# Kernel tuning notes

Hardware: AMD Instinct MI355X
Metric: run time of the kernel (lower is better)

## Reference

```python
import jax, jax.numpy as jnp
import numpy as np


def crf_log_likelihood(logits, tags, mask, transitions, start_trans, end_trans):
    """AllenNLP-style linear-chain CRF log-likelihood, summed over the batch.
    logits: [B,T,K] float, tags: [B,T] int, mask: [B,T] float (1=valid).
    include_start_end_transitions=True.
    """
    B, T, K = logits.shape
    lt = jnp.transpose(logits, (1, 0, 2))          # [T,B,K]
    mt = jnp.transpose(mask, (1, 0))               # [T,B]
    tt = jnp.transpose(tags, (1, 0))               # [T,B]

    # ---- partition function (forward algorithm) ----
    alpha0 = start_trans + lt[0]                   # [B,K]

    def part_step(alpha, xs):
        emit, m = xs                               # emit [B,K], m [B]
        # inner[b,i,j] = alpha[b,i] + transitions[i,j] + emit[b,j]
        inner = alpha[:, :, None] + emit[:, None, :] + transitions[None, :, :]
        new_alpha = jax.nn.logsumexp(inner, axis=1)
        alpha = new_alpha * m[:, None] + alpha * (1.0 - m[:, None])
        return alpha, None

    alpha, _ = jax.lax.scan(part_step, alpha0, (lt[1:], mt[1:]))
    log_denominator = jax.nn.logsumexp(alpha + end_trans, axis=1)  # [B]

    # ---- joint (gold-path) score ----
    score0 = start_trans[tt[0]]                    # [B]

    def joint_step(score, xs):
        cur, nxt, emit, m_cur, m_nxt = xs
        trans_s = transitions[cur, nxt]                                   # [B]
        emit_s = jnp.take_along_axis(emit, cur[:, None], axis=1)[:, 0]    # [B]
        return score + trans_s * m_nxt + emit_s * m_cur, None

    score, _ = jax.lax.scan(joint_step, score0,
                            (tt[:-1], tt[1:], lt[:-1], mt[:-1], mt[1:]))
    last_idx = (jnp.sum(mt, axis=0) - 1.0).astype(jnp.int32)              # [B]
    last_tags = tt[last_idx, jnp.arange(B)]                               # [B]
    last_emit = jnp.take_along_axis(lt[-1], last_tags[:, None], axis=1)[:, 0]
    score = score + end_trans[last_tags] + last_emit * mt[-1]
    return jnp.sum(score - log_denominator)


def setup_inputs() -> dict:
    key = jax.random.key(0)
    ks = jax.random.split(key, 6)
    B, T, D, K = 64, 512, 768, 21
    vectors = jax.random.normal(ks[0], (B, T, D), dtype=jnp.float32)
    targets = jax.random.randint(ks[1], (B, T), 0, K, dtype=jnp.int32)
    mask = jnp.ones((B, T), dtype=jnp.int32)
    # Linear(input_dim, n_classes)
    W = jax.random.normal(ks[2], (K, D), dtype=jnp.float32) * (1.0 / np.sqrt(D))
    b = jax.random.normal(ks[3], (K,), dtype=jnp.float32) * 0.01
    transitions = jax.random.normal(ks[4], (K, K), dtype=jnp.float32) * 0.1
    se = jax.random.normal(ks[5], (2, K), dtype=jnp.float32) * 0.1
    return {"vectors": vectors, "targets": targets, "mask": mask,
            "W": W, "b": b, "transitions": transitions,
            "start_trans": se[0], "end_trans": se[1]}


def reference(vectors, targets, mask, W, b, transitions, start_trans, end_trans):
    logits = jnp.einsum('btd,kd->btk', vectors, W) + b     # proj
    maskf = mask.astype(logits.dtype)
    ll = crf_log_likelihood(logits, targets, maskf, transitions, start_trans, end_trans)
    loss = -ll / jnp.sum(maskf)
    return loss, logits
```

## Files before the change

kernel.cpp:

```cpp
#include <hip/hip_runtime.h>

#define B_ 64
#define T_ 512
#define D_ 768
#define K_ 21
#define NCHUNK 32
#define CLEN 16
#define GSTRIDE 448
#define LOG21 3.0445224377234229965f
#define WSTRIDE 776
#define ASTRIDE 136

using f16x8 = __attribute__((ext_vector_type(8))) _Float16;
using h16x4 = __attribute__((ext_vector_type(4))) _Float16;
using f32x4 = __attribute__((ext_vector_type(4))) float;

__global__ __launch_bounds__(256) void proj_kernel(
    const float* __restrict__ A,
    const float* __restrict__ W,
    const float* __restrict__ bias,
    float* __restrict__ out)
{
    __shared__ _Float16 Wh[K_ * WSTRIDE];
    __shared__ _Float16 Ah[2][64 * ASTRIDE];
    const int tid  = threadIdx.x;
    const int lane = tid & 63;
    const int w    = tid >> 6;
    const int m    = lane & 15;
    const int quad = lane >> 4;
    const size_t row0 = (size_t)blockIdx.x * 64;

    {
        const float4* Wg = (const float4*)W;
        for (int i = tid; i < K_ * D_ / 4; i += 256) {
            const float4 v = Wg[i];
            const int fi = i * 4;
            const int r = fi / D_;
            const int c = fi - r * D_;
            h16x4 h;
            h[0] = (_Float16)v.x; h[1] = (_Float16)v.y;
            h[2] = (_Float16)v.z; h[3] = (_Float16)v.w;
            *(h16x4*)(&Wh[r * WSTRIDE + c]) = h;
        }
    }

    float4 pf[8];
    #pragma unroll
    for (int j = 0; j < 8; ++j) {
        const int i = tid + j * 256;
        const int r = i >> 5, c4 = i & 31;
        pf[j] = *(const float4*)(A + (row0 + r) * D_ + c4 * 4);
    }
    #pragma unroll
    for (int j = 0; j < 8; ++j) {
        const int i = tid + j * 256;
        const int r = i >> 5, c4 = i & 31;
        h16x4 h;
        h[0] = (_Float16)pf[j].x; h[1] = (_Float16)pf[j].y;
        h[2] = (_Float16)pf[j].z; h[3] = (_Float16)pf[j].w;
        *(h16x4*)(&Ah[0][r * ASTRIDE + c4 * 4]) = h;
    }
    __syncthreads();

    f32x4 acc0 = {0.f, 0.f, 0.f, 0.f};
    f32x4 acc1 = {0.f, 0.f, 0.f, 0.f};
    const int n1 = (16 + m < K_) ? 16 + m : K_ - 1;

    for (int kt = 0; kt < 6; ++kt) {
        if (kt < 5) {
            #pragma unroll
            for (int j = 0; j < 8; ++j) {
                const int i = tid + j * 256;
                const int r = i >> 5, c4 = i & 31;
                pf[j] = *(const float4*)(A + (row0 + r) * D_ + (kt + 1) * 128 + c4 * 4);
            }
        }
        const _Float16* Ab = Ah[kt & 1];
        #pragma unroll
        for (int s = 0; s < 4; ++s) {
            const f16x8 af = *(const f16x8*)(&Ab[(w * 16 + m) * ASTRIDE + s * 32 + quad * 8]);
            const f16x8 bf = *(const f16x8*)(&Wh[m * WSTRIDE + kt * 128 + s * 32 + quad * 8]);
            const f16x8 cf = *(const f16x8*)(&Wh[n1 * WSTRIDE + kt * 128 + s * 32 + quad * 8]);
            acc0 = __builtin_amdgcn_mfma_f32_16x16x32_f16(af, bf, acc0, 0, 0, 0);
            acc1 = __builtin_amdgcn_mfma_f32_16x16x32_f16(af, cf, acc1, 0, 0, 0);
        }
        if (kt < 5) {
            _Float16* Aw = Ah[(kt + 1) & 1];
            #pragma unroll
            for (int j = 0; j < 8; ++j) {
                const int i = tid + j * 256;
                const int r = i >> 5, c4 = i & 31;
                h16x4 h;
                h[0] = (_Float16)pf[j].x; h[1] = (_Float16)pf[j].y;
                h[2] = (_Float16)pf[j].z; h[3] = (_Float16)pf[j].w;
                *(h16x4*)(&Aw[r * ASTRIDE + c4 * 4]) = h;
            }
        }
        __syncthreads();
    }

    const size_t rbase = row0 + w * 16 + quad * 4;
    {
        const float bb = bias[m];
        float* o = out + 1 + rbase * K_ + m;
        #pragma unroll
        for (int r = 0; r < 4; ++r) o[(size_t)r * K_] = acc0[r] + bb;
    }
    const int col2 = 16 + m;
    if (col2 < K_) {
        const float bb = bias[col2];
        float* o = out + 1 + rbase * K_ + col2;
        #pragma unroll
        for (int r = 0; r < 4; ++r) o[(size_t)r * K_] = acc1[r] + bb;
    }
}

__global__ __launch_bounds__(64, 1) void chunk_kernel(
    const float* __restrict__ outF,
    const int*   __restrict__ mask,
    const float* __restrict__ trans,
    float* __restrict__ G,
    float* __restrict__ SC)
{
    __shared__ float M0[441], M1[441];
    __shared__ float sET[441];
    __shared__ float em[CLEN * K_];
    __shared__ float smx[CLEN];
    __shared__ int   smask[CLEN];

    const int c = blockIdx.x;
    const int b = blockIdx.y;
    const int lane = threadIdx.x;
    const int t0 = c * CLEN + 1;
    const int nst = min(CLEN, T_ - t0);
    const int i_ = lane / 3;
    const int jg = lane - i_ * 3;
    const bool act = lane < 63;

    const float* lg = outF + 1 + (size_t)b * T_ * K_;
    for (int idx = lane; idx < nst * K_; idx += 64) em[idx] = lg[t0 * K_ + idx];
    if (lane < nst) smask[lane] = mask[b * T_ + t0 + lane];
    for (int idx = lane; idx < 441; idx += 64) {
        M0[idx] = (idx % 22 == 0) ? 1.0f : 0.0f;
        sET[idx] = __expf(trans[idx]);
    }
    __syncthreads();

    if (lane < nst) {
        float mx = -1e30f;
        for (int j = 0; j < K_; ++j) mx = fmaxf(mx, em[lane * K_ + j]);
        smx[lane] = mx;
    }
    __syncthreads();
    for (int idx = lane; idx < nst * K_; idx += 64)
        em[idx] = __expf(em[idx] - smx[idx / K_]) * (1.0f / 21.0f);

    float ETc[K_ * 7];
    if (act) {
        #pragma unroll
        for (int mm = 0; mm < K_; ++mm) {
            #pragma unroll
            for (int q = 0; q < 7; ++q)
                ETc[mm * 7 + q] = sET[mm * K_ + jg * 7 + q];
        }
    }
    __syncthreads();

    int cur = 0;
    for (int s = 0; s < nst; ++s) {
        if (smask[s] != 0) {
            const float* Mr = cur ? M1 : M0;
            float*       Mw = cur ? M0 : M1;
            float facc[7] = {0.f,0.f,0.f,0.f,0.f,0.f,0.f};
            if (act) {
                #pragma unroll
                for (int mm = 0; mm < K_; ++mm) {
                    const float lm = Mr[i_ * K_ + mm];
                    #pragma unroll
                    for (int q = 0; q < 7; ++q)
                        facc[q] = fmaf(lm, ETc[mm * 7 + q], facc[q]);
                }
            }
            __syncthreads();
            if (act) {
                #pragma unroll
                for (int q = 0; q < 7; ++q)
                    Mw[i_ * K_ + jg * 7 + q] = facc[q] * em[s * K_ + jg * 7 + q];
            }
            __syncthreads();
            cur ^= 1;
        }
    }

    float* Gc = G + (size_t)(b * NCHUNK + c) * GSTRIDE;
    const float* Mf = cur ? M1 : M0;
    for (int idx = lane; idx < 441; idx += 64) Gc[idx] = Mf[idx];
    if (lane == 0) {
        float sc = 0.0f;
        for (int s = 0; s < nst; ++s)
            if (smask[s] != 0) sc += smx[s] + LOG21;
        SC[b * NCHUNK + c] = sc;
    }
}

__global__ __launch_bounds__(256) void scan_kernel(
    const float* __restrict__ outF,
    const int*   __restrict__ tags,
    const int*   __restrict__ mask,
    const float* __restrict__ trans,
    const float* __restrict__ startT,
    const float* __restrict__ endT,
    const float* __restrict__ G,
    const float* __restrict__ SC,
    float* __restrict__ ll,
    float* __restrict__ msum)
{
    __shared__ float sG[NCHUNK * GSTRIDE];
    __shared__ float sm[T_];
    __shared__ int   st[T_];
    __shared__ float part[8];
    const int tid = threadIdx.x;
    const int lane = tid & 63;
    const int w = tid >> 6;
    const int b = blockIdx.x;
    const float* lg = outF + 1 + (size_t)b * T_ * K_;

    {
        const float4* Gf4 = (const float4*)(G + (size_t)b * NCHUNK * GSTRIDE);
        float4* dst = (float4*)sG;
        for (int i = tid; i < NCHUNK * GSTRIDE / 4; i += 256) dst[i] = Gf4[i];
    }
    for (int t = tid; t < T_; t += 256) {
        sm[t] = (float)mask[b * T_ + t];
        st[t] = tags[b * T_ + t];
    }
    __syncthreads();

    float logZ = 0.0f;
    if (w == 0) {
        const float scv = (lane < NCHUNK) ? SC[b * NCHUNK + lane] : 0.0f;
        const int jc = min(lane, K_ - 1);
        float v = (lane < K_) ? __expf(startT[lane] + lg[lane]) : 0.0f;
        float C = 0.0f;
        for (int c = 0; c < NCHUNK; ++c) {
            const float* Gc = sG + c * GSTRIDE;
            float a0 = 0.f, a1 = 0.f, a2 = 0.f;
            #pragma unroll
            for (int i = 0; i < K_; i += 3) {
                a0 = fmaf(__shfl(v, i,     64), Gc[i * K_ + jc],       a0);
                a1 = fmaf(__shfl(v, i + 1, 64), Gc[(i + 1) * K_ + jc], a1);
                a2 = fmaf(__shfl(v, i + 2, 64), Gc[(i + 2) * K_ + jc], a2);
            }
            const float s = a0 + a1 + a2;
            const float s0 = __shfl(s, 0, 64);
            v = s / s0;
            C += __logf(s0) + __shfl(scv, c, 64);
        }
        float term = (lane < K_) ? v * __expf(endT[lane]) : 0.0f;
        #pragma unroll
        for (int off = 16; off >= 1; off >>= 1) term += __shfl_xor(term, off, 64);
        term += __shfl_xor(term, 32, 64);
        logZ = C + __logf(term);
    } else {
        float sc = 0.0f, ms = 0.0f;
        for (int t = tid - 64; t < T_; t += 192) {
            const float mt = sm[t];
            ms += mt;
            if (t < T_ - 1) {
                const int ct = st[t], nt2 = st[t + 1];
                sc += trans[ct * K_ + nt2] * sm[t + 1] + lg[t * K_ + ct] * mt;
            }
        }
        #pragma unroll
        for (int off = 32; off >= 1; off >>= 1) {
            sc += __shfl_xor(sc, off, 64);
            ms += __shfl_xor(ms, off, 64);
        }
        if (lane == 0) { part[w] = sc; part[4 + w] = ms; }
    }
    __syncthreads();

    if (tid == 0) {
        float sc = part[1] + part[2] + part[3];
        float ms = part[5] + part[6] + part[7];
        const int lastIdx = (int)ms - 1;
        const int lastTag = st[lastIdx];
        sc += startT[st[0]] + endT[lastTag] + lg[(T_ - 1) * K_ + lastTag] * sm[T_ - 1];
        ll[b]   = sc - logZ;
        msum[b] = ms;
    }
}

__global__ __launch_bounds__(64) void fin_kernel(
    const float* __restrict__ ll, const float* __restrict__ msum,
    float* __restrict__ outF)
{
    const int lane = threadIdx.x;
    float l = ll[lane];
    float m = msum[lane];
    #pragma unroll
    for (int off = 32; off >= 1; off >>= 1) {
        l += __shfl_xor(l, off, 64);
        m += __shfl_xor(m, off, 64);
    }
    if (lane == 0) outF[0] = -l / m;
}

__global__ __launch_bounds__(64) void crf_kernel(
    const float* __restrict__ outF,
    const int*   __restrict__ tags,
    const int*   __restrict__ mask,
    const float* __restrict__ trans,
    const float* __restrict__ startT,
    const float* __restrict__ endT,
    float* __restrict__ ws)
{
    __shared__ float se[T_ * K_];
    __shared__ float sm[T_];
    __shared__ int   st[T_];
    const int b = blockIdx.x;
    const int lane = threadIdx.x;

    const float* lg = outF + 1 + (size_t)b * T_ * K_;
    for (int i = lane; i < T_ * K_; i += 64) se[i] = lg[i];
    for (int t = lane; t < T_; t += 64) {
        sm[t] = (float)mask[b * T_ + t];
        st[t] = tags[b * T_ + t];
    }
    __syncthreads();

    const int jc = lane < K_ ? lane : K_ - 1;
    float ET[K_];
    #pragma unroll
    for (int i = 0; i < K_; ++i) ET[i] = __expf(trans[i * K_ + jc]);

    float a0   = startT[jc] + se[jc];
    float r0   = __shfl(a0, 0, 64);
    float aRel = a0 - r0;
    float C    = r0;

    for (int t = 1; t < T_; ++t) {
        if (sm[t] != 0.0f) {
            float e = __expf(aRel);
            float s = 0.0f;
            #pragma unroll
            for (int i = 0; i < K_; ++i)
                s = fmaf(__shfl(e, i, 64), ET[i], s);
            float raw = __logf(s) + se[t * K_ + jc];
            float rr  = __shfl(raw, 0, 64);
            aRel = raw - rr;
            C   += rr;
        }
    }

    float contrib = (lane < K_) ? __expf(aRel + endT[jc]) : 0.0f;
    #pragma unroll
    for (int off = 32; off >= 1; off >>= 1) contrib += __shfl_xor(contrib, off, 64);
    const float logZ = C + __logf(contrib);

    float sc = 0.0f, ms = 0.0f;
    for (int t = lane; t < T_; t += 64) {
        const float mt = sm[t];
        ms += mt;
        if (t < T_ - 1) {
            const int ct = st[t], nt2 = st[t + 1];
            sc += trans[ct * K_ + nt2] * sm[t + 1] + se[t * K_ + ct] * mt;
        }
    }
    #pragma unroll
    for (int off = 32; off >= 1; off >>= 1) {
        sc += __shfl_xor(sc, off, 64);
        ms += __shfl_xor(ms, off, 64);
    }
    if (lane == 0) {
        const int lastIdx = (int)ms - 1;
        const int lastTag = st[lastIdx];
        sc += startT[st[0]] + endT[lastTag] + se[(T_ - 1) * K_ + lastTag] * sm[T_ - 1];
        ws[b]      = sc - logZ;
        ws[B_ + b] = ms;
    }
}

extern "C" void kernel_launch(void* const* d_in, const int* in_sizes, int n_in,
                              void* d_out, int out_size, void* d_ws, size_t ws_size,
                              hipStream_t stream) {
    const float* A     = (const float*)d_in[0];
    const int*   tags  = (const int*)  d_in[1];
    const int*   mask  = (const int*)  d_in[2];
    const float* W     = (const float*)d_in[3];
    const float* bias  = (const float*)d_in[4];
    const float* trans = (const float*)d_in[5];
    const float* stT   = (const float*)d_in[6];
    const float* enT   = (const float*)d_in[7];
    float* outF = (float*)d_out;
    float* ws   = (float*)d_ws;

    proj_kernel<<<512, 256, 0, stream>>>(A, W, bias, outF);

    const size_t gFloats  = (size_t)B_ * NCHUNK * GSTRIDE;
    const size_t scOff    = gFloats;
    const size_t llOff    = gFloats + (size_t)B_ * NCHUNK;
    const size_t msOff    = llOff + B_;
    const size_t needBytes = (msOff + B_) * sizeof(float);

    if (ws_size >= needBytes) {
        float* G   = ws;
        float* SC  = ws + scOff;
        float* llp = ws + llOff;
        float* msv = ws + msOff;
        chunk_kernel<<<dim3(NCHUNK, B_), 64, 0, stream>>>(outF, mask, trans, G, SC);
        scan_kernel<<<B_, 256, 0, stream>>>(outF, tags, mask, trans, stT, enT, G, SC, llp, msv);
        fin_kernel<<<1, 64, 0, stream>>>(llp, msv, outF);
    } else {
        crf_kernel<<<B_, 64, 0, stream>>>(outF, tags, mask, trans, stT, enT, ws);
        fin_kernel<<<1, 64, 0, stream>>>(ws, ws + B_, outF);
    }
}
```

Measured before the change: 207.0 us.

## Fuse CRF chunk transfer-matrix computation into projection epilogue and fold final reduction

Each projection wave computes its 16-timestep CRF transfer matrix directly from the logits it just produced. The logits are staged in reused LDS, so the separate chunk kernel and its global reload of logits go away. Synchronization inside the chunk recurrence becomes wave-local waits instead of block barriers. The final loss reduction moves into the scan kernel through an atomic last-block counter, which removes the fin kernel launch. The cost is extra LDS, extra work in the projection epilogue, and a chunk grouping shifted by one timestep, which makes the projection kernel heavier.

```diff
diff --git a/kernel.cpp b/kernel.cpp
--- a/kernel.cpp
+++ b/kernel.cpp
@@ -5,30 +5,52 @@
 #define D_ 768
 #define K_ 21
 #define NCHUNK 32
-#define CLEN 16
 #define GSTRIDE 448
 #define LOG21 3.0445224377234229965f
 #define WSTRIDE 776
 #define ASTRIDE 136
 
+#define WAVE_SYNC() asm volatile("s_waitcnt lgkmcnt(0)" ::: "memory")
+
 using f16x8 = __attribute__((ext_vector_type(8))) _Float16;
 using h16x4 = __attribute__((ext_vector_type(4))) _Float16;
 using f32x4 = __attribute__((ext_vector_type(4))) float;
 
-__global__ __launch_bounds__(256) void proj_kernel(
+__global__ __launch_bounds__(256, 2) void proj_chunk_kernel(
     const float* __restrict__ A,
     const float* __restrict__ W,
     const float* __restrict__ bias,
-    float* __restrict__ out)
+    const int*   __restrict__ mask,
+    const float* __restrict__ trans,
+    float* __restrict__ out,
+    float* __restrict__ G,
+    float* __restrict__ SC,
+    int*   __restrict__ cnt)
 {
     __shared__ _Float16 Wh[K_ * WSTRIDE];
     __shared__ _Float16 Ah[2][64 * ASTRIDE];
+    __shared__ float    sET[441];
     const int tid  = threadIdx.x;
     const int lane = tid & 63;
     const int w    = tid >> 6;
     const int m    = lane & 15;
     const int quad = lane >> 4;
     const size_t row0 = (size_t)blockIdx.x * 64;
+    const bool gmode = (G != nullptr);
+
+    if (gmode && blockIdx.x == 0 && tid == 0) *cnt = 0;
+
+    const int b     = blockIdx.x >> 3;
+    const int chunk = ((blockIdx.x & 7) << 2) + w;
+    const int t0    = chunk * 16;
+
+    unsigned int mbits = 0;
+    if (gmode) {
+        const int mv = (lane < 16) ? mask[b * T_ + t0 + lane] : 0;
+        const unsigned long long mb = __ballot(mv != 0);
+        mbits = (unsigned int)(mb & 0xFFFFull);
+        if (chunk == 0) mbits &= ~1u;
+    }
 
     {
         const float4* Wg = (const float4*)W;
@@ -43,6 +65,7 @@
             *(h16x4*)(&Wh[r * WSTRIDE + c]) = h;
         }
     }
+    for (int i = tid; i < 441; i += 256) sET[i] = __expf(trans[i]);
 
     float4 pf[8];
     #pragma unroll
@@ -99,62 +122,53 @@
         __syncthreads();
     }
 
+    float* const cb  = reinterpret_cast<float*>(&Ah[0][0]) + w * 1280;
+    float* const M0p = cb;
+    float* const M1p = cb + 441;
+    float* const em  = cb + 882;
+    float* const smx = cb + 1218;
+
     const size_t rbase = row0 + w * 16 + quad * 4;
     {
         const float bb = bias[m];
         float* o = out + 1 + rbase * K_ + m;
         #pragma unroll
-        for (int r = 0; r < 4; ++r) o[(size_t)r * K_] = acc0[r] + bb;
+        for (int r = 0; r < 4; ++r) {
+            const float v = acc0[r] + bb;
+            o[(size_t)r * K_] = v;
+            if (gmode) em[(quad * 4 + r) * K_ + m] = v;
+        }
     }
     const int col2 = 16 + m;
     if (col2 < K_) {
         const float bb = bias[col2];
         float* o = out + 1 + rbase * K_ + col2;
         #pragma unroll
-        for (int r = 0; r < 4; ++r) o[(size_t)r * K_] = acc1[r] + bb;
-    }
-}
-
-__global__ __launch_bounds__(64, 1) void chunk_kernel(
-    const float* __restrict__ outF,
-    const int*   __restrict__ mask,
-    const float* __restrict__ trans,
-    float* __restrict__ G,
-    float* __restrict__ SC)
-{
-    __shared__ float M0[441], M1[441];
-    __shared__ float sET[441];
-    __shared__ float em[CLEN * K_];
-    __shared__ float smx[CLEN];
-    __shared__ int   smask[CLEN];
-
-    const int c = blockIdx.x;
-    const int b = blockIdx.y;
-    const int lane = threadIdx.x;
-    const int t0 = c * CLEN + 1;
-    const int nst = min(CLEN, T_ - t0);
-    const int i_ = lane / 3;
-    const int jg = lane - i_ * 3;
-    const bool act = lane < 63;
-
-    const float* lg = outF + 1 + (size_t)b * T_ * K_;
-    for (int idx = lane; idx < nst * K_; idx += 64) em[idx] = lg[t0 * K_ + idx];
-    if (lane < nst) smask[lane] = mask[b * T_ + t0 + lane];
-    for (int idx = lane; idx < 441; idx += 64) {
-        M0[idx] = (idx % 22 == 0) ? 1.0f : 0.0f;
-        sET[idx] = __expf(trans[idx]);
-    }
-    __syncthreads();
-
-    if (lane < nst) {
+        for (int r = 0; r < 4; ++r) {
+            const float v = acc1[r] + bb;
+            o[(size_t)r * K_] = v;
+            if (gmode) em[(quad * 4 + r) * K_ + col2] = v;
+        }
+    }
+    if (!gmode) return;
+    WAVE_SYNC();
+
+    if (lane < 16) {
         float mx = -1e30f;
+        #pragma unroll
         for (int j = 0; j < K_; ++j) mx = fmaxf(mx, em[lane * K_ + j]);
         smx[lane] = mx;
     }
-    __syncthreads();
-    for (int idx = lane; idx < nst * K_; idx += 64)
-        em[idx] = __expf(em[idx] - smx[idx / K_]) * (1.0f / 21.0f);
-
+    WAVE_SYNC();
+    #pragma unroll
+    for (int ii = 0; ii < 6; ++ii) {
+        const int idx = lane + ii * 64;
+        if (idx < 336) em[idx] = __expf(em[idx] - smx[idx / K_]) * (1.0f / 21.0f);
+    }
+
+    const int  i_  = lane / 3;
+    const int  jg  = lane - i_ * 3;
+    const bool act = lane < 63;
     float ETc[K_ * 7];
     if (act) {
         #pragma unroll
@@ -164,15 +178,17 @@
                 ETc[mm * 7 + q] = sET[mm * K_ + jg * 7 + q];
         }
     }
-    __syncthreads();
+    for (int idx = lane; idx < 441; idx += 64)
+        M0p[idx] = (idx % 22 == 0) ? 1.0f : 0.0f;
+    WAVE_SYNC();
 
     int cur = 0;
-    for (int s = 0; s < nst; ++s) {
-        if (smask[s] != 0) {
-            const float* Mr = cur ? M1 : M0;
-            float*       Mw = cur ? M0 : M1;
-            float facc[7] = {0.f,0.f,0.f,0.f,0.f,0.f,0.f};
+    for (int s = 0; s < 16; ++s) {
+        if ((mbits >> s) & 1u) {
+            const float* Mr = cur ? M1p : M0p;
+            float*       Mw = cur ? M0p : M1p;
             if (act) {
+                float facc[7] = {0.f,0.f,0.f,0.f,0.f,0.f,0.f};
                 #pragma unroll
                 for (int mm = 0; mm < K_; ++mm) {
                     const float lm = Mr[i_ * K_ + mm];
@@ -180,30 +196,26 @@
                     for (int q = 0; q < 7; ++q)
                         facc[q] = fmaf(lm, ETc[mm * 7 + q], facc[q]);
                 }
-            }
-            __syncthreads();
-            if (act) {
                 #pragma unroll
                 for (int q = 0; q < 7; ++q)
                     Mw[i_ * K_ + jg * 7 + q] = facc[q] * em[s * K_ + jg * 7 + q];
             }
-            __syncthreads();
+            WAVE_SYNC();
             cur ^= 1;
         }
     }
 
-    float* Gc = G + (size_t)(b * NCHUNK + c) * GSTRIDE;
-    const float* Mf = cur ? M1 : M0;
+    float scv = (lane < 16 && ((mbits >> lane) & 1u)) ? smx[lane] + LOG21 : 0.0f;
+    #pragma unroll
+    for (int off = 8; off >= 1; off >>= 1) scv += __shfl_xor(scv, off, 64);
+
+    const float* Mf = cur ? M1p : M0p;
+    float* Gc = G + (size_t)(b * NCHUNK + chunk) * GSTRIDE;
     for (int idx = lane; idx < 441; idx += 64) Gc[idx] = Mf[idx];
-    if (lane == 0) {
-        float sc = 0.0f;
-        for (int s = 0; s < nst; ++s)
-            if (smask[s] != 0) sc += smx[s] + LOG21;
-        SC[b * NCHUNK + c] = sc;
-    }
+    if (lane == 0) SC[b * NCHUNK + chunk] = scv;
 }
 
-__global__ __launch_bounds__(256) void scan_kernel(
+__global__ __launch_bounds__(256) void scan_fin_kernel(
     const float* __restrict__ outF,
     const int*   __restrict__ tags,
     const int*   __restrict__ mask,
@@ -213,12 +225,15 @@
     const float* __restrict__ G,
     const float* __restrict__ SC,
     float* __restrict__ ll,
-    float* __restrict__ msum)
+    float* __restrict__ msum,
+    int*   __restrict__ cnt,
+    float* __restrict__ outW)
 {
     __shared__ float sG[NCHUNK * GSTRIDE];
     __shared__ float sm[T_];
     __shared__ int   st[T_];
     __shared__ float part[8];
+    __shared__ int   lastF;
     const int tid = threadIdx.x;
     const int lane = tid & 63;
     const int w = tid >> 6;
@@ -288,6 +303,21 @@
         sc += startT[st[0]] + endT[lastTag] + lg[(T_ - 1) * K_ + lastTag] * sm[T_ - 1];
         ll[b]   = sc - logZ;
         msum[b] = ms;
+        __threadfence();
+        lastF = (atomicAdd(cnt, 1) == B_ - 1) ? 1 : 0;
+    }
+    __syncthreads();
+
+    if (lastF != 0 && w == 0) {
+        __threadfence();
+        float l  = ll[lane];
+        float mm = msum[lane];
+        #pragma unroll
+        for (int off = 32; off >= 1; off >>= 1) {
+            l  += __shfl_xor(l,  off, 64);
+            mm += __shfl_xor(mm, off, 64);
+        }
+        if (lane == 0) outW[0] = -l / mm;
     }
 }
 
@@ -395,23 +425,23 @@
     float* outF = (float*)d_out;
     float* ws   = (float*)d_ws;
 
-    proj_kernel<<<512, 256, 0, stream>>>(A, W, bias, outF);
-
-    const size_t gFloats  = (size_t)B_ * NCHUNK * GSTRIDE;
-    const size_t scOff    = gFloats;
-    const size_t llOff    = gFloats + (size_t)B_ * NCHUNK;
-    const size_t msOff    = llOff + B_;
-    const size_t needBytes = (msOff + B_) * sizeof(float);
+    const size_t gFloats = (size_t)B_ * NCHUNK * GSTRIDE;
+    const size_t scOff   = gFloats;
+    const size_t llOff   = scOff + (size_t)B_ * NCHUNK;
+    const size_t msOff   = llOff + B_;
+    const size_t cntOff  = msOff + B_;
+    const size_t needBytes = cntOff * sizeof(float) + sizeof(int);
 
     if (ws_size >= needBytes) {
         float* G   = ws;
         float* SC  = ws + scOff;
         float* llp = ws + llOff;
         float* msv = ws + msOff;
-        chunk_kernel<<<dim3(NCHUNK, B_), 64, 0, stream>>>(outF, mask, trans, G, SC);
-        scan_kernel<<<B_, 256, 0, stream>>>(outF, tags, mask, trans, stT, enT, G, SC, llp, msv);
-        fin_kernel<<<1, 64, 0, stream>>>(llp, msv, outF);
+        int*   cnt = (int*)(ws + cntOff);
+        proj_chunk_kernel<<<512, 256, 0, stream>>>(A, W, bias, mask, trans, outF, G, SC, cnt);
+        scan_fin_kernel<<<B_, 256, 0, stream>>>(outF, tags, mask, trans, stT, enT, G, SC, llp, msv, cnt, outF);
     } else {
+        proj_chunk_kernel<<<512, 256, 0, stream>>>(A, W, bias, mask, trans, outF, nullptr, nullptr, nullptr);
         crf_kernel<<<B_, 64, 0, stream>>>(outF, tags, mask, trans, stT, enT, ws);
         fin_kernel<<<1, 64, 0, stream>>>(ws, ws + B_, outF);
     }
```

After: 202.1 us, median of 2. 2.4% less time.
